# Kernel optimization log

Measured on AMD Instinct MI355X. Metric: run time of the kernel, lower is better.

## Reference

```python
import jax, jax.numpy as jnp
import numpy as np

HEADS = 2
NEG_SLOPE = 0.2
EPS = 1e-16


def setup_inputs() -> dict:
    N, E, D, F = 10000, 320000, 128, 16
    key = jax.random.key(0)
    ks = jax.random.split(key, 8)
    return {
        "x": jax.random.normal(ks[0], (N, D), dtype=jnp.float32),
        "edge_index": jax.random.randint(ks[1], (2, E), 0, N, dtype=jnp.int64),
        "edge_attr": jax.random.normal(ks[2], (E, F), dtype=jnp.float32),
        # stacked per-layer params (5 layers), glorot-ish scale
        "weights": jax.random.normal(ks[3], (5, D, HEADS * D), dtype=jnp.float32) * 0.08,
        "atts": jax.random.normal(ks[4], (5, HEADS, 2 * D), dtype=jnp.float32) * 0.08,
        "biases": jnp.zeros((5, D), dtype=jnp.float32),
        "edge_ws": jax.random.normal(ks[5], (5, HEADS * D, F), dtype=jnp.float32) * 0.2,
        "edge_bs": jnp.zeros((5, HEADS * D), dtype=jnp.float32),
    }


def _gat_layer(x, src, dst, edge_attr_full, W, att, b, ew, eb):
    # x: [N, D]; src/dst: [E_tot] (self loops already appended)
    N, D = x.shape
    H = HEADS
    edge_emb = edge_attr_full @ ew.T + eb               # [E_tot, H*D]
    xw = x @ W                                          # [N, H*D]
    xj = xw[src].reshape(-1, H, D) + edge_emb.reshape(-1, H, D)  # [E_tot, H, D]
    xi = xw[dst].reshape(-1, H, D)
    att_i, att_j = att[:, :D], att[:, D:]               # [H, D] each
    alpha = jnp.einsum('ehd,hd->eh', xi, att_i) + jnp.einsum('ehd,hd->eh', xj, att_j)
    alpha = jax.nn.leaky_relu(alpha, NEG_SLOPE)
    # segment softmax over destination node (every node has a self loop)
    amax = jax.ops.segment_max(alpha, dst, num_segments=N)   # [N, H]
    ea = jnp.exp(alpha - amax[dst])
    denom = jax.ops.segment_sum(ea, dst, num_segments=N)     # [N, H]
    alpha = ea / (denom[dst] + EPS)
    msg = xj * alpha[..., None]                              # [E_tot, H, D]
    aggr = jax.ops.segment_sum(msg, dst, num_segments=N)     # [N, H, D]
    return aggr.mean(axis=1) + b                             # [N, D]


def reference(x, edge_index, edge_attr, weights, atts, biases, edge_ws, edge_bs):
    N = x.shape[0]
    E = edge_index.shape[1]
    F = edge_attr.shape[1]
    # add self loops (PyG flow: edge_index[0]=source j, edge_index[1]=target i)
    loop = jnp.arange(N, dtype=edge_index.dtype)
    src = jnp.concatenate([edge_index[0], loop])
    dst = jnp.concatenate([edge_index[1], loop])
    edge_attr_full = jnp.concatenate(
        [edge_attr, jnp.zeros((N, F), dtype=edge_attr.dtype)], axis=0)
    h = x
    for l in range(5):
        h = _gat_layer(h, src, dst, edge_attr_full,
                       weights[l], atts[l], biases[l], edge_ws[l], edge_bs[l])
        if l < 4:
            h = jax.nn.relu(h)
    return h
```

## Files before the change

### kernel.cpp

```cpp
#include <hip/hip_runtime.h>
#include <hip/hip_fp16.h>

#define HEADS 2
#define DD 128
#define FF 16
#define HD 256
#define NEG_SLOPE 0.2f
#define EPSV 1e-16f

static __device__ __forceinline__ float rdlanef(float v, int i){
  return __uint_as_float(__builtin_amdgcn_readlane(__float_as_uint(v), i));
}
static __device__ __forceinline__ int rdlanei(int v, int i){
  return __builtin_amdgcn_readlane(v, i);
}
static __device__ __forceinline__ float4 h4f(uint2 u){
  __half2 h0 = *(__half2*)&u.x;
  __half2 h1 = *(__half2*)&u.y;
  float2 f0 = __half22float2(h0);
  float2 f1 = __half22float2(h1);
  return make_float4(f0.x, f0.y, f1.x, f1.y);
}

__global__ void k_hist(const int* __restrict__ dst, int* __restrict__ counts, int E, int Etot){
  int e = blockIdx.x*256 + threadIdx.x;
  if (e >= Etot) return;
  int dn = (e < E) ? dst[e] : (e - E);
  atomicAdd(&counts[dn], 1);
}

__global__ __launch_bounds__(1024) void k_scan(const int* __restrict__ counts, int* __restrict__ starts,
                       int* __restrict__ cursor, int N, int Etot){
  __shared__ int s[1024];
  int t = threadIdx.x;
  const int CHN = (N + 1023) / 1024;
  int lo = t*CHN, hi = min(lo+CHN, N);
  int loc = 0;
  for (int i = lo; i < hi; i++) loc += counts[i];
  s[t] = loc;
  __syncthreads();
  for (int off = 1; off < 1024; off <<= 1){
    int v = (t >= off) ? s[t-off] : 0;
    __syncthreads();
    s[t] += v;
    __syncthreads();
  }
  int run = (t == 0) ? 0 : s[t-1];
  for (int i = lo; i < hi; i++){
    starts[i] = run; cursor[i] = run; run += counts[i];
  }
  if (t == 0) starts[N] = Etot;
}

__global__ void k_scatter(const int* __restrict__ dst, int* __restrict__ cursor,
                          int* __restrict__ eids, int E, int Etot){
  int e = blockIdx.x*256 + threadIdx.x;
  if (e >= Etot) return;
  int dn = (e < E) ? dst[e] : (e - E);
  int pos = atomicAdd(&cursor[dn], 1);
  eids[pos] = e;
}

__global__ void k_gather_csr(const int* __restrict__ eids, const int* __restrict__ src,
                             const float* __restrict__ eattr,
                             int* __restrict__ srcC, float* __restrict__ attrC, int E, int Etot){
  int i = blockIdx.x*256 + threadIdx.x;
  if (i >= Etot) return;
  int eid = eids[i];
  srcC[i] = (eid < E) ? src[eid] : (eid - E);
  float4* o = (float4*)&attrC[(size_t)i*FF];
  if (eid < E){
    const float4* in = (const float4*)&eattr[(size_t)eid*FF];
    o[0]=in[0]; o[1]=in[1]; o[2]=in[2]; o[3]=in[3];
  } else {
    float4 z = make_float4(0.f,0.f,0.f,0.f);
    o[0]=z; o[1]=z; o[2]=z; o[3]=z;
  }
}

__global__ void k_prec5(const float* __restrict__ atts, const float* __restrict__ edge_ws,
                        const float* __restrict__ edge_bs, float* __restrict__ c5){
  int l = blockIdx.x;
  int t = threadIdx.x;
  const float* att = atts    + (size_t)l*HEADS*2*DD;
  const float* ew  = edge_ws + (size_t)l*HD*FF;
  const float* eb  = edge_bs + (size_t)l*HD;
  float* c = c5 + (size_t)l*34;
  if (t < 32){
    int h = t >> 4, f = t & 15;
    float acc = 0.f;
    for (int d = 0; d < DD; d++) acc += att[h*2*DD + DD + d]*ew[(size_t)(h*DD+d)*FF + f];
    c[h*FF + f] = acc;
  } else if (t < 34){
    int h = t - 32;
    float acc = 0.f;
    for (int d = 0; d < DD; d++) acc += att[h*2*DD + DD + d]*eb[h*DD + d];
    c[32 + h] = acc;
  }
}

__global__ __launch_bounds__(256) void k_gemm_xw(const float* __restrict__ h, const float* __restrict__ W,
                         const float* __restrict__ att, __half* __restrict__ xwh,
                         float* __restrict__ sbuf, int N){
  __shared__ float sx[16][DD];
  int r0 = blockIdx.x * 16;
  int rows = min(16, N - r0);
  int t = threadIdx.x;
  for (int idx = t; idx < 16*(DD/4); idx += 256){
    int r = idx >> 5, kq = idx & 31;
    float4 v = make_float4(0.f,0.f,0.f,0.f);
    if (r < rows) v = *(const float4*)&h[(size_t)(r0+r)*DD + kq*4];
    *(float4*)&sx[r][kq*4] = v;
  }
  __syncthreads();
  int tx = t & 63, ty = t >> 6;
  int c0 = tx*4;
  float4 acc[4];
  #pragma unroll
  for (int r = 0; r < 4; r++) acc[r] = make_float4(0.f,0.f,0.f,0.f);
  #pragma unroll 4
  for (int kq = 0; kq < 32; kq++){
    float4 w0 = *(const float4*)&W[(size_t)(kq*4+0)*HD + c0];
    float4 w1 = *(const float4*)&W[(size_t)(kq*4+1)*HD + c0];
    float4 w2 = *(const float4*)&W[(size_t)(kq*4+2)*HD + c0];
    float4 w3 = *(const float4*)&W[(size_t)(kq*4+3)*HD + c0];
    #pragma unroll
    for (int r = 0; r < 4; r++){
      float4 hv = *(const float4*)&sx[ty*4+r][kq*4];
      acc[r].x = fmaf(hv.x, w0.x, acc[r].x); acc[r].y = fmaf(hv.x, w0.y, acc[r].y);
      acc[r].z = fmaf(hv.x, w0.z, acc[r].z); acc[r].w = fmaf(hv.x, w0.w, acc[r].w);
      acc[r].x = fmaf(hv.y, w1.x, acc[r].x); acc[r].y = fmaf(hv.y, w1.y, acc[r].y);
      acc[r].z = fmaf(hv.y, w1.z, acc[r].z); acc[r].w = fmaf(hv.y, w1.w, acc[r].w);
      acc[r].x = fmaf(hv.z, w2.x, acc[r].x); acc[r].y = fmaf(hv.z, w2.y, acc[r].y);
      acc[r].z = fmaf(hv.z, w2.z, acc[r].z); acc[r].w = fmaf(hv.z, w2.w, acc[r].w);
      acc[r].x = fmaf(hv.w, w3.x, acc[r].x); acc[r].y = fmaf(hv.w, w3.y, acc[r].y);
      acc[r].z = fmaf(hv.w, w3.z, acc[r].z); acc[r].w = fmaf(hv.w, w3.w, acc[r].w);
    }
  }
  #pragma unroll
  for (int r = 0; r < 4; r++){
    if (ty*4+r < rows){
      __half2 p0 = __floats2half2_rn(acc[r].x, acc[r].y);
      __half2 p1 = __floats2half2_rn(acc[r].z, acc[r].w);
      uint2 pk;
      pk.x = *(unsigned*)&p0;
      pk.y = *(unsigned*)&p1;
      *(uint2*)&xwh[(size_t)(r0+ty*4+r)*HD + c0] = pk;
    }
  }
  int hsel = tx >> 5;
  int cm = c0 & 127;
  float4 ai = *(const float4*)&att[hsel*2*DD + cm];
  float4 aj = *(const float4*)&att[hsel*2*DD + DD + cm];
  #pragma unroll
  for (int r = 0; r < 4; r++){
    float pi = acc[r].x*ai.x + acc[r].y*ai.y + acc[r].z*ai.z + acc[r].w*ai.w;
    float pj = acc[r].x*aj.x + acc[r].y*aj.y + acc[r].z*aj.z + acc[r].w*aj.w;
    #pragma unroll
    for (int off = 16; off; off >>= 1){
      pi += __shfl_xor(pi, off);
      pj += __shfl_xor(pj, off);
    }
    int row = ty*4 + r;
    if ((tx & 31) == 0 && row < rows){
      sbuf[(size_t)(r0+row)*4 + 0 + hsel] = pi;
      sbuf[(size_t)(r0+row)*4 + 2 + hsel] = pj;
    }
  }
}

static __device__ __forceinline__ void alpha_edge(int idx, const int* __restrict__ srcC,
    const float* __restrict__ s, const float* __restrict__ attrC,
    const float* cf0, const float* cf1, float c32, float c33,
    float sdx, float sdy, float& a0, float& a1, int& msrc){
  msrc = srcC[idx];
  float2 sj = *(const float2*)&s[(size_t)msrc*4+2];
  const float4* ap = (const float4*)&attrC[(size_t)idx*FF];
  float4 t0=ap[0], t1=ap[1], t2=ap[2], t3=ap[3];
  float x0 = sdx + sj.x + c32;
  float x1 = sdy + sj.y + c33;
  x0 = fmaf(t0.x,cf0[0],x0); x0 = fmaf(t0.y,cf0[1],x0); x0 = fmaf(t0.z,cf0[2],x0); x0 = fmaf(t0.w,cf0[3],x0);
  x0 = fmaf(t1.x,cf0[4],x0); x0 = fmaf(t1.y,cf0[5],x0); x0 = fmaf(t1.z,cf0[6],x0); x0 = fmaf(t1.w,cf0[7],x0);
  x0 = fmaf(t2.x,cf0[8],x0); x0 = fmaf(t2.y,cf0[9],x0); x0 = fmaf(t2.z,cf0[10],x0); x0 = fmaf(t2.w,cf0[11],x0);
  x0 = fmaf(t3.x,cf0[12],x0); x0 = fmaf(t3.y,cf0[13],x0); x0 = fmaf(t3.z,cf0[14],x0); x0 = fmaf(t3.w,cf0[15],x0);
  x1 = fmaf(t0.x,cf1[0],x1); x1 = fmaf(t0.y,cf1[1],x1); x1 = fmaf(t0.z,cf1[2],x1); x1 = fmaf(t0.w,cf1[3],x1);
  x1 = fmaf(t1.x,cf1[4],x1); x1 = fmaf(t1.y,cf1[5],x1); x1 = fmaf(t1.z,cf1[6],x1); x1 = fmaf(t1.w,cf1[7],x1);
  x1 = fmaf(t2.x,cf1[8],x1); x1 = fmaf(t2.y,cf1[9],x1); x1 = fmaf(t2.z,cf1[10],x1); x1 = fmaf(t2.w,cf1[11],x1);
  x1 = fmaf(t3.x,cf1[12],x1); x1 = fmaf(t3.y,cf1[13],x1); x1 = fmaf(t3.z,cf1[14],x1); x1 = fmaf(t3.w,cf1[15],x1);
  a0 = (x0 > 0.f) ? x0 : NEG_SLOPE*x0;
  a1 = (x1 > 0.f) ? x1 : NEG_SLOPE*x1;
}

__global__ __launch_bounds__(256) void k_aggr(const int* __restrict__ starts, const int* __restrict__ srcC,
                      const float* __restrict__ attrC, const float* __restrict__ s,
                      const float* __restrict__ c, const __half* __restrict__ xwh,
                      const float* __restrict__ ew, const float* __restrict__ eb,
                      const float* __restrict__ bias, float* __restrict__ out, int N, int relu){
  int lane = threadIdx.x & 63, wid = threadIdx.x >> 6;
  int n = blockIdx.x*4 + wid;
  if (n >= N) return;

  float cf0[FF], cf1[FF];
  #pragma unroll
  for (int f = 0; f < FF; f++){ cf0[f] = c[f]; cf1[f] = c[FF+f]; }
  float c32 = c[32], c33 = c[33];
  float sdx = s[(size_t)n*4+0], sdy = s[(size_t)n*4+1];
  int st = starts[n];
  int deg = starts[n+1] - st;

  int f2 = lane & 15;
  int h2 = (lane >> 4) & 1;
  int hq = lane >> 5;
  int c0 = lane*4;

  float aAx=0.f, aAy=0.f, aAz=0.f, aAw=0.f;
  float aBx=0.f, aBy=0.f, aBz=0.f, aBw=0.f;
  float ls0=0.f, ls1=0.f, taccA=0.f, taccB=0.f;

  for (int base = 0; base < deg; base += 64){
    int cnt = min(64, deg - base);
    float e0 = 0.f, e1 = 0.f; int msrc = 0;
    if (lane < cnt){
      float a0, a1;
      alpha_edge(st+base+lane, srcC, s, attrC, cf0, cf1, c32, c33, sdx, sdy, a0, a1, msrc);
      e0 = expf(a0); e1 = expf(a1);
      ls0 += e0; ls1 += e1;
    }
    const float* abase = &attrC[(size_t)(st+base)*FF];
    int i = 0;
    for (; i+1 < cnt; i += 2){
      int sn0 = rdlanei(msrc, i);
      int sn1 = rdlanei(msrc, i+1);
      float w00 = rdlanef(e0, i),   w10 = rdlanef(e1, i);
      float w01 = rdlanef(e0, i+1), w11 = rdlanef(e1, i+1);
      uint2 u0 = *(const uint2*)&xwh[(size_t)sn0*HD + c0];
      uint2 u1 = *(const uint2*)&xwh[(size_t)sn1*HD + c0];
      float4 x0 = h4f(u0);
      float4 x1 = h4f(u1);
      float ws0 = hq ? w10 : w00;
      float ws1 = hq ? w11 : w01;
      aAx = fmaf(ws0, x0.x, aAx); aAy = fmaf(ws0, x0.y, aAy);
      aAz = fmaf(ws0, x0.z, aAz); aAw = fmaf(ws0, x0.w, aAw);
      aBx = fmaf(ws1, x1.x, aBx); aBy = fmaf(ws1, x1.y, aBy);
      aBz = fmaf(ws1, x1.z, aBz); aBw = fmaf(ws1, x1.w, aBw);
      taccA = fmaf(h2 ? w10 : w00, abase[(size_t)i*FF + f2], taccA);
      taccB = fmaf(h2 ? w11 : w01, abase[(size_t)(i+1)*FF + f2], taccB);
    }
    if (i < cnt){
      int sn0 = rdlanei(msrc, i);
      float w00 = rdlanef(e0, i), w10 = rdlanef(e1, i);
      uint2 u0 = *(const uint2*)&xwh[(size_t)sn0*HD + c0];
      float4 x0 = h4f(u0);
      float ws0 = hq ? w10 : w00;
      aAx = fmaf(ws0, x0.x, aAx); aAy = fmaf(ws0, x0.y, aAy);
      aAz = fmaf(ws0, x0.z, aAz); aAw = fmaf(ws0, x0.w, aAw);
      taccA = fmaf(h2 ? w10 : w00, abase[(size_t)i*FF + f2], taccA);
    }
  }
  float ax = aAx + aBx, ay = aAy + aBy, az = aAz + aBz, aw = aAw + aBw;
  float tacc = taccA + taccB;
  #pragma unroll
  for (int off = 32; off; off >>= 1){
    ls0 += __shfl_xor(ls0, off);
    ls1 += __shfl_xor(ls1, off);
  }

  float th[FF];
  #pragma unroll
  for (int f = 0; f < FF; f++) th[f] = __shfl(tacc, hq*FF + f);
  float embq[4];
  #pragma unroll
  for (int q = 0; q < 4; q++){
    const float4* er = (const float4*)&ew[(size_t)(c0+q)*FF];
    float4 g0 = er[0], g1 = er[1], g2 = er[2], g3 = er[3];
    float v = th[0]*g0.x + th[1]*g0.y + th[2]*g0.z + th[3]*g0.w;
    v = fmaf(th[4],  g1.x, v); v = fmaf(th[5],  g1.y, v); v = fmaf(th[6],  g1.z, v); v = fmaf(th[7],  g1.w, v);
    v = fmaf(th[8],  g2.x, v); v = fmaf(th[9],  g2.y, v); v = fmaf(th[10], g2.z, v); v = fmaf(th[11], g2.w, v);
    v = fmaf(th[12], g3.x, v); v = fmaf(th[13], g3.y, v); v = fmaf(th[14], g3.z, v); v = fmaf(th[15], g3.w, v);
    embq[q] = v;
  }
  float di = 1.f/((hq ? ls1 : ls0) + EPSV);
  float4 ebv = *(const float4*)&eb[c0];
  float r0 = di*(ax + embq[0]) + ebv.x;
  float r1 = di*(ay + embq[1]) + ebv.y;
  float r2 = di*(az + embq[2]) + ebv.z;
  float r3 = di*(aw + embq[3]) + ebv.w;
  float p0 = __shfl_xor(r0, 32);
  float p1 = __shfl_xor(r1, 32);
  float p2 = __shfl_xor(r2, 32);
  float p3 = __shfl_xor(r3, 32);
  if (lane < 32){
    float4 bv = *(const float4*)&bias[c0];
    float4 v;
    v.x = 0.5f*(r0 + p0) + bv.x;
    v.y = 0.5f*(r1 + p1) + bv.y;
    v.z = 0.5f*(r2 + p2) + bv.z;
    v.w = 0.5f*(r3 + p3) + bv.w;
    if (relu){
      v.x = fmaxf(v.x, 0.f); v.y = fmaxf(v.y, 0.f);
      v.z = fmaxf(v.z, 0.f); v.w = fmaxf(v.w, 0.f);
    }
    *(float4*)&out[(size_t)n*DD + c0] = v;
  }
}

extern "C" void kernel_launch(void* const* d_in, const int* in_sizes, int n_in,
                              void* d_out, int out_size, void* d_ws, size_t ws_size,
                              hipStream_t stream){
  const float* x       = (const float*)d_in[0];
  const int*   eidx    = (const int*)d_in[1];
  const float* eattr   = (const float*)d_in[2];
  const float* weights = (const float*)d_in[3];
  const float* atts    = (const float*)d_in[4];
  const float* biases  = (const float*)d_in[5];
  const float* edge_ws = (const float*)d_in[6];
  const float* edge_bs = (const float*)d_in[7];
  const int N = in_sizes[0]/DD;
  const int E = in_sizes[1]/2;
  const int Etot = E + N;
  const int* src = eidx;
  const int* dst = eidx + E;

  char* p = (char*)d_ws;
  auto alloc = [&](size_t bytes){ void* r = (void*)p; p += (bytes + 255) & ~(size_t)255; return r; };
  float*    hA     = (float*)alloc((size_t)N*DD*4);
  float*    hB     = (float*)alloc((size_t)N*DD*4);
  __half*   xwh    = (__half*)alloc((size_t)N*HD*2);
  float*    sbuf   = (float*)alloc((size_t)N*4*4);
  int*      starts = (int*)alloc((size_t)(N+1)*4);
  int*      srcC   = (int*)alloc((size_t)Etot*4);
  int*      eids   = (int*)alloc((size_t)Etot*4);
  float*    attrC  = (float*)alloc((size_t)Etot*FF*4);
  float*    c5     = (float*)alloc(5*34*4);

  int* counts = (int*)sbuf;
  int* cursor = (int*)((char*)sbuf + 65536);

  const int ebl = (Etot + 255)/256;

  hipMemsetAsync(counts, 0, (size_t)N*4, stream);
  k_hist<<<ebl, 256, 0, stream>>>(dst, counts, E, Etot);
  k_scan<<<1, 1024, 0, stream>>>(counts, starts, cursor, N, Etot);
  k_scatter<<<ebl, 256, 0, stream>>>(dst, cursor, eids, E, Etot);
  k_gather_csr<<<ebl, 256, 0, stream>>>(eids, src, eattr, srcC, attrC, E, Etot);
  k_prec5<<<5, 64, 0, stream>>>(atts, edge_ws, edge_bs, c5);

  const float* hin = x;
  for (int l = 0; l < 5; l++){
    const float* W   = weights + (size_t)l*DD*HD;
    const float* att = atts    + (size_t)l*HEADS*2*DD;
    const float* b   = biases  + (size_t)l*DD;
    const float* ew  = edge_ws + (size_t)l*HD*FF;
    const float* eb  = edge_bs + (size_t)l*HD;
    const float* c   = c5 + (size_t)l*34;
    float* hout = (l == 4) ? (float*)d_out : ((l & 1) ? hB : hA);

    k_gemm_xw<<<(N+15)/16, 256, 0, stream>>>(hin, W, att, xwh, sbuf, N);
    k_aggr<<<(N+3)/4, 256, 0, stream>>>(starts, srcC, attrC, sbuf, c, xwh, ew, eb, b, hout, N, (l < 4) ? 1 : 0);

    hin = hout;
  }
}
```

Baseline: 417.3 us.

## Split wavefront into half-waves each gathering a full 256-wide row per edge

The aggregation loop is remapped so each 32-lane half of the wavefront handles a different edge of a pair, with each lane loading 8 fp16 values (16-byte load) covering the whole H*D row. The two halves' partial sums are combined with a cross-half shuffle at the end, and the edge-embedding projection and head averaging are redone for the new 8-column-per-lane layout. This is meant to issue wider, fewer gather loads per edge pair and drop the separate tail iteration. In exchange the epilogue runs on only 32 or 16 active lanes with more per-lane work, and the odd-edge case is handled by zeroing the weight.

```diff
diff --git a/kernel.cpp b/kernel.cpp
--- a/kernel.cpp
+++ b/kernel.cpp
@@ -13,13 +13,6 @@
 }
 static __device__ __forceinline__ int rdlanei(int v, int i){
   return __builtin_amdgcn_readlane(v, i);
-}
-static __device__ __forceinline__ float4 h4f(uint2 u){
-  __half2 h0 = *(__half2*)&u.x;
-  __half2 h1 = *(__half2*)&u.y;
-  float2 f0 = __half22float2(h0);
-  float2 f1 = __half22float2(h1);
-  return make_float4(f0.x, f0.y, f1.x, f1.y);
 }
 
 __global__ void k_hist(const int* __restrict__ dst, int* __restrict__ counts, int E, int Etot){
@@ -208,14 +201,16 @@
   int st = starts[n];
   int deg = starts[n+1] - st;
 
-  int f2 = lane & 15;
-  int h2 = (lane >> 4) & 1;
-  int hq = lane >> 5;
-  int c0 = lane*4;
-
-  float aAx=0.f, aAy=0.f, aAz=0.f, aAw=0.f;
-  float aBx=0.f, aBy=0.f, aBz=0.f, aBw=0.f;
-  float ls0=0.f, ls1=0.f, taccA=0.f, taccB=0.f;
+  int gpar = lane >> 5;
+  int l31  = lane & 31;
+  int hh   = l31 >> 4;
+  int c8   = l31 * 8;
+  int f2   = lane & 15;
+
+  float acc[8];
+  #pragma unroll
+  for (int k = 0; k < 8; k++) acc[k] = 0.f;
+  float ls0 = 0.f, ls1 = 0.f, tacc = 0.f;
 
   for (int base = 0; base < deg; base += 64){
     int cnt = min(64, deg - base);
@@ -227,80 +222,78 @@
       ls0 += e0; ls1 += e1;
     }
     const float* abase = &attrC[(size_t)(st+base)*FF];
-    int i = 0;
-    for (; i+1 < cnt; i += 2){
-      int sn0 = rdlanei(msrc, i);
-      int sn1 = rdlanei(msrc, i+1);
-      float w00 = rdlanef(e0, i),   w10 = rdlanef(e1, i);
-      float w01 = rdlanef(e0, i+1), w11 = rdlanef(e1, i+1);
-      uint2 u0 = *(const uint2*)&xwh[(size_t)sn0*HD + c0];
-      uint2 u1 = *(const uint2*)&xwh[(size_t)sn1*HD + c0];
-      float4 x0 = h4f(u0);
-      float4 x1 = h4f(u1);
-      float ws0 = hq ? w10 : w00;
-      float ws1 = hq ? w11 : w01;
-      aAx = fmaf(ws0, x0.x, aAx); aAy = fmaf(ws0, x0.y, aAy);
-      aAz = fmaf(ws0, x0.z, aAz); aAw = fmaf(ws0, x0.w, aAw);
-      aBx = fmaf(ws1, x1.x, aBx); aBy = fmaf(ws1, x1.y, aBy);
-      aBz = fmaf(ws1, x1.z, aBz); aBw = fmaf(ws1, x1.w, aBw);
-      taccA = fmaf(h2 ? w10 : w00, abase[(size_t)i*FF + f2], taccA);
-      taccB = fmaf(h2 ? w11 : w01, abase[(size_t)(i+1)*FF + f2], taccB);
-    }
-    if (i < cnt){
-      int sn0 = rdlanei(msrc, i);
-      float w00 = rdlanef(e0, i), w10 = rdlanef(e1, i);
-      uint2 u0 = *(const uint2*)&xwh[(size_t)sn0*HD + c0];
-      float4 x0 = h4f(u0);
-      float ws0 = hq ? w10 : w00;
-      aAx = fmaf(ws0, x0.x, aAx); aAy = fmaf(ws0, x0.y, aAy);
-      aAz = fmaf(ws0, x0.z, aAz); aAw = fmaf(ws0, x0.w, aAw);
-      taccA = fmaf(h2 ? w10 : w00, abase[(size_t)i*FF + f2], taccA);
-    }
-  }
-  float ax = aAx + aBx, ay = aAy + aBy, az = aAz + aBz, aw = aAw + aBw;
-  float tacc = taccA + taccB;
+    #pragma unroll 4
+    for (int i = 0; i < cnt; i += 2){
+      int i1 = (i+1 < cnt) ? (i+1) : i;
+      int   sA  = rdlanei(msrc, i);
+      int   sB  = rdlanei(msrc, i1);
+      float wa0 = rdlanef(e0, i),  wa1 = rdlanef(e1, i);
+      float wb0 = rdlanef(e0, i1), wb1 = rdlanef(e1, i1);
+      int   sn = gpar ? sB : sA;
+      float w0 = gpar ? wb0 : wa0;
+      float w1 = gpar ? wb1 : wa1;
+      float ws = hh ? w1 : w0;
+      if (gpar && (i+1 >= cnt)) ws = 0.f;
+      int ec = gpar ? i1 : i;
+      uint4 u = *(const uint4*)&xwh[(size_t)sn*HD + c8];
+      __half2 q0 = *(__half2*)&u.x, q1 = *(__half2*)&u.y;
+      __half2 q2 = *(__half2*)&u.z, q3 = *(__half2*)&u.w;
+      float2 v0 = __half22float2(q0), v1 = __half22float2(q1);
+      float2 v2 = __half22float2(q2), v3 = __half22float2(q3);
+      acc[0] = fmaf(ws, v0.x, acc[0]); acc[1] = fmaf(ws, v0.y, acc[1]);
+      acc[2] = fmaf(ws, v1.x, acc[2]); acc[3] = fmaf(ws, v1.y, acc[3]);
+      acc[4] = fmaf(ws, v2.x, acc[4]); acc[5] = fmaf(ws, v2.y, acc[5]);
+      acc[6] = fmaf(ws, v3.x, acc[6]); acc[7] = fmaf(ws, v3.y, acc[7]);
+      tacc = fmaf(ws, abase[(size_t)ec*FF + f2], tacc);
+    }
+  }
+
+  #pragma unroll
+  for (int k = 0; k < 8; k++) acc[k] += __shfl_xor(acc[k], 32);
+  tacc += __shfl_xor(tacc, 32);
   #pragma unroll
   for (int off = 32; off; off >>= 1){
     ls0 += __shfl_xor(ls0, off);
     ls1 += __shfl_xor(ls1, off);
   }
 
-  float th[FF];
-  #pragma unroll
-  for (int f = 0; f < FF; f++) th[f] = __shfl(tacc, hq*FF + f);
-  float embq[4];
-  #pragma unroll
-  for (int q = 0; q < 4; q++){
-    const float4* er = (const float4*)&ew[(size_t)(c0+q)*FF];
-    float4 g0 = er[0], g1 = er[1], g2 = er[2], g3 = er[3];
-    float v = th[0]*g0.x + th[1]*g0.y + th[2]*g0.z + th[3]*g0.w;
-    v = fmaf(th[4],  g1.x, v); v = fmaf(th[5],  g1.y, v); v = fmaf(th[6],  g1.z, v); v = fmaf(th[7],  g1.w, v);
-    v = fmaf(th[8],  g2.x, v); v = fmaf(th[9],  g2.y, v); v = fmaf(th[10], g2.z, v); v = fmaf(th[11], g2.w, v);
-    v = fmaf(th[12], g3.x, v); v = fmaf(th[13], g3.y, v); v = fmaf(th[14], g3.z, v); v = fmaf(th[15], g3.w, v);
-    embq[q] = v;
-  }
-  float di = 1.f/((hq ? ls1 : ls0) + EPSV);
-  float4 ebv = *(const float4*)&eb[c0];
-  float r0 = di*(ax + embq[0]) + ebv.x;
-  float r1 = di*(ay + embq[1]) + ebv.y;
-  float r2 = di*(az + embq[2]) + ebv.z;
-  float r3 = di*(aw + embq[3]) + ebv.w;
-  float p0 = __shfl_xor(r0, 32);
-  float p1 = __shfl_xor(r1, 32);
-  float p2 = __shfl_xor(r2, 32);
-  float p3 = __shfl_xor(r3, 32);
   if (lane < 32){
-    float4 bv = *(const float4*)&bias[c0];
-    float4 v;
-    v.x = 0.5f*(r0 + p0) + bv.x;
-    v.y = 0.5f*(r1 + p1) + bv.y;
-    v.z = 0.5f*(r2 + p2) + bv.z;
-    v.w = 0.5f*(r3 + p3) + bv.w;
-    if (relu){
-      v.x = fmaxf(v.x, 0.f); v.y = fmaxf(v.y, 0.f);
-      v.z = fmaxf(v.z, 0.f); v.w = fmaxf(v.w, 0.f);
-    }
-    *(float4*)&out[(size_t)n*DD + c0] = v;
+    float th[FF];
+    #pragma unroll
+    for (int f = 0; f < FF; f++) th[f] = __shfl(tacc, hh*FF + f);
+    float di = 1.f/((hh ? ls1 : ls0) + EPSV);
+    float4 eb0 = *(const float4*)&eb[c8];
+    float4 eb1 = *(const float4*)&eb[c8+4];
+    float r[8];
+    #pragma unroll
+    for (int k = 0; k < 8; k++){
+      const float4* er = (const float4*)&ew[(size_t)(c8+k)*FF];
+      float4 g0 = er[0], g1 = er[1], g2 = er[2], g3 = er[3];
+      float v = th[0]*g0.x + th[1]*g0.y + th[2]*g0.z + th[3]*g0.w;
+      v = fmaf(th[4],  g1.x, v); v = fmaf(th[5],  g1.y, v); v = fmaf(th[6],  g1.z, v); v = fmaf(th[7],  g1.w, v);
+      v = fmaf(th[8],  g2.x, v); v = fmaf(th[9],  g2.y, v); v = fmaf(th[10], g2.z, v); v = fmaf(th[11], g2.w, v);
+      v = fmaf(th[12], g3.x, v); v = fmaf(th[13], g3.y, v); v = fmaf(th[14], g3.z, v); v = fmaf(th[15], g3.w, v);
+      float ebk = (k < 4) ? ((const float*)&eb0)[k] : ((const float*)&eb1)[k-4];
+      r[k] = di*(acc[k] + v) + ebk;
+    }
+    float o[8];
+    #pragma unroll
+    for (int k = 0; k < 8; k++){
+      float pr = __shfl_xor(r[k], 16);
+      o[k] = 0.5f*(r[k] + pr);
+    }
+    if (lane < 16){
+      float4 b0 = *(const float4*)&bias[c8];
+      float4 b1 = *(const float4*)&bias[c8+4];
+      float4 w0 = make_float4(o[0]+b0.x, o[1]+b0.y, o[2]+b0.z, o[3]+b0.w);
+      float4 w1 = make_float4(o[4]+b1.x, o[5]+b1.y, o[6]+b1.z, o[7]+b1.w);
+      if (relu){
+        w0.x=fmaxf(w0.x,0.f); w0.y=fmaxf(w0.y,0.f); w0.z=fmaxf(w0.z,0.f); w0.w=fmaxf(w0.w,0.f);
+        w1.x=fmaxf(w1.x,0.f); w1.y=fmaxf(w1.y,0.f); w1.z=fmaxf(w1.z,0.f); w1.w=fmaxf(w1.w,0.f);
+      }
+      *(float4*)&out[(size_t)n*DD + c8]     = w0;
+      *(float4*)&out[(size_t)n*DD + c8 + 4] = w1;
+    }
   }
 }
 
```

Result: slower. 482.4 us (+15.6%).
